# Kernel tuning notes

Hardware: AMD Instinct MI355X
Metric: run time of the kernel (lower is better)

## Reference

```python
import jax, jax.numpy as jnp
import numpy as np

C_CURV = 0.001
L = 10
N = 16
OMEGA = 1.0
EPS = 1e-6


def _fnmap(x, a0, a, b):
    # x: [M, C]; radial Fourier gate
    r = jnp.maximum(jnp.linalg.norm(x, axis=1, keepdims=True), EPS)  # [M,1]
    n = jnp.arange(1, N + 1, dtype=x.dtype)[None, :]                 # [1,N]
    angle = OMEGA * (r * n)                                          # [M,N]
    f_r = a0 + jnp.cos(angle) @ a[:, None] + jnp.sin(angle) @ b[:, None]  # [M,1]
    return f_r * x


def _log_map_origin(x, c):
    sc = jnp.sqrt(c)
    rn = jnp.maximum(jnp.linalg.norm(x, axis=1, keepdims=True), EPS)
    arg = jnp.minimum(sc * rn, 1.0 - 1e-5)
    return (jnp.arctanh(arg) / (sc * rn)) * x


def _exp_map_origin(v, c):
    sc = jnp.sqrt(c)
    rn = jnp.maximum(jnp.linalg.norm(v, axis=1, keepdims=True), EPS)
    return (jnp.tanh(sc * rn) / (sc * rn)) * v


def setup_inputs() -> dict:
    key = jax.random.key(0)
    ks = jax.random.split(key, 8)
    B, C, H, W = 32, 256, 64, 64
    x = jax.random.normal(ks[0], (B, C, H, W), dtype=jnp.float32) * 0.1
    inp = {
        "x": x,
        "a0_1": jnp.ones((1,), jnp.float32),
        "a_1": jax.random.normal(ks[1], (N,), jnp.float32) * 0.02,
        "b_1": jax.random.normal(ks[2], (N,), jnp.float32) * 0.02,
        "a0_2": jnp.ones((1,), jnp.float32),
        "a_2": jax.random.normal(ks[3], (N,), jnp.float32) * 0.02,
        "b_2": jax.random.normal(ks[4], (N,), jnp.float32) * 0.02,
        "phi": jax.random.normal(ks[5], (C,), jnp.float32) * 0.02,
        "alpha": jnp.ones((1,), jnp.float32),
        "beta": jnp.zeros((1,), jnp.float32),
    }
    return inp


def reference(x, a0_1, a_1, b_1, a0_2, a_2, b_2, phi, alpha, beta):
    B, C, H, W = x.shape
    h0 = jnp.transpose(x, (0, 2, 3, 1)).reshape(-1, C)  # [B*H*W, C]
    u = _log_map_origin(h0, C_CURV)
    u1 = _fnmap(u, a0_1, a_1, b_1)
    U = jnp.fft.rfft(u1, axis=1)                         # [M, C//2+1]
    ang = L * phi
    Hf = jax.lax.complex(jnp.cos(ang), jnp.sin(ang))     # [C]
    V = U * Hf[None, : U.shape[-1]]
    v0 = jnp.fft.irfft(V, n=C, axis=1)
    v1 = _fnmap(v0, a0_2, a_2, b_2)
    y = _exp_map_origin(v1, C_CURV)
    out = alpha * y + beta * h0
    return jnp.transpose(out.reshape(B, H, W, C), (0, 3, 1, 2))
```

## Files before the change

### kernel.cpp

```cpp
#include <hip/hip_runtime.h>
#include <math.h>

typedef __attribute__((ext_vector_type(8))) unsigned short ushort8;
typedef __attribute__((ext_vector_type(8))) __bf16 bf16x8;
typedef __attribute__((ext_vector_type(4))) float f32x4;

constexpr int   CDIM  = 256;
constexpr int   HWSP  = 4096;
constexpr int   PPB   = 64;
constexpr float SQRTC = 0.031622776601683794f;
constexpr float EPSR  = 1e-6f;

__device__ inline unsigned short f2bf(float x) {
    unsigned int u = __float_as_uint(x);
    u += 0x7FFFu + ((u >> 16) & 1u);
    return (unsigned short)(u >> 16);
}
__device__ inline float bf2f(unsigned short v) {
    return __uint_as_float(((unsigned int)v) << 16);
}

__global__ void build_w_kernel(const float* __restrict__ phi,
                               float* __restrict__ w) {
    const int d = threadIdx.x;
    const float step = 6.283185307179586f / 256.0f;
    double s = 0.0;
    for (int k = 1; k <= 127; ++k) {
        int kd = (k * d) & 255;
        float ang = 10.0f * phi[k] + step * (float)kd;
        s += 2.0 * (double)cosf(ang);
    }
    s += (double)cosf(10.0f * phi[0]);
    double c128 = (double)cosf(10.0f * phi[128]);
    s += (d & 1) ? -c128 : c128;
    w[d] = (float)(s * (1.0 / 256.0));
}

__global__ void build_wbf_kernel(const float* __restrict__ w,
                                 unsigned short* __restrict__ wbf) {
    const int j = blockIdx.x;
    const int c = threadIdx.x;
    wbf[j * CDIM + c] = f2bf(w[(j - c) & 255]);
}

__device__ inline float fourier_gate(float r, float A0,
                                     const float* __restrict__ a,
                                     const float* __restrict__ b) {
    float sn, cs;
    sincosf(r, &sn, &cs);
    float c = cs, s = sn, f = A0;
    #pragma unroll
    for (int n = 0; n < 16; ++n) {
        f = fmaf(a[n], c, f);
        f = fmaf(b[n], s, f);
        float c2 = fmaf(c, cs, -s * sn);
        float s2 = fmaf(s, cs,  c * sn);
        c = c2; s = s2;
    }
    return f;
}

__global__ __launch_bounds__(256, 3)
void fused_mfma(const float* __restrict__ x,
                const float* __restrict__ a0_1, const float* __restrict__ a1,
                const float* __restrict__ b1,
                const float* __restrict__ a0_2, const float* __restrict__ a2,
                const float* __restrict__ b2,
                const float* __restrict__ alpha, const float* __restrict__ beta,
                const unsigned short* __restrict__ wbf,
                float* __restrict__ out) {
    __shared__ __align__(16) unsigned short Xl[PPB][CDIM];
    __shared__ float ns[4][PPB];
    __shared__ float sc2[4][PPB];
    __shared__ float s1buf[PPB];
    __shared__ float sobuf[PPB];

    const int t  = threadIdx.x;
    const int l  = t & 63;
    const int g  = t >> 6;
    const int b  = blockIdx.x >> 6;
    const int s0 = (blockIdx.x & 63) * PPB;
    const float* xb = x + (size_t)b * CDIM * HWSP + s0;

    {
        const int p   = l;
        const int swz = (p & 7) << 3;
        float n0sq = 0.f;
        #pragma unroll
        for (int k = 0; k < 8; ++k) {
            const int ch0 = (g + 4 * k) * 8;
            float v[8];
            #pragma unroll
            for (int j = 0; j < 8; ++j)
                v[j] = xb[(size_t)(ch0 + j) * HWSP + p];
            ushort8 u;
            #pragma unroll
            for (int j = 0; j < 8; ++j) {
                n0sq = fmaf(v[j], v[j], n0sq);
                u[j] = f2bf(v[j]);
            }
            *reinterpret_cast<ushort8*>(&Xl[p][ch0 ^ swz]) = u;
        }
        ns[g][p] = n0sq;
    }
    __syncthreads();

    if (t < PPB) {
        float nsq = ns[0][t] + ns[1][t] + ns[2][t] + ns[3][t];
        float n0  = sqrtf(nsq);
        float rn0 = fmaxf(n0, EPSR);
        float arg = fminf(SQRTC * rn0, 1.0f - 1e-5f);
        float ls  = atanhf(arg) / (SQRTC * rn0);
        float r1  = fmaxf(ls * n0, EPSR);
        s1buf[t]  = ls * fourier_gate(r1, a0_1[0], a1, b1);
    }

    const int lr = l & 15;
    const int lk = l >> 4;
    const int jbase = g * 64;
    f32x4 acc[4][4];
    #pragma unroll
    for (int m = 0; m < 4; ++m)
        #pragma unroll
        for (int n = 0; n < 4; ++n)
            acc[m][n] = f32x4{0.f, 0.f, 0.f, 0.f};

    #pragma unroll
    for (int ks = 0; ks < 8; ++ks) {
        const int kb = ks * 32 + lk * 8;
        bf16x8 af[4], bfr[4];
        #pragma unroll
        for (int m = 0; m < 4; ++m) {
            const int row = jbase + m * 16 + lr;
            af[m] = __builtin_bit_cast(bf16x8,
                *reinterpret_cast<const ushort8*>(&wbf[row * CDIM + kb]));
        }
        #pragma unroll
        for (int n = 0; n < 4; ++n) {
            const int pos = n * 16 + lr;
            const int ch  = kb ^ ((pos & 7) << 3);
            bfr[n] = __builtin_bit_cast(bf16x8,
                *reinterpret_cast<const ushort8*>(&Xl[pos][ch]));
        }
        #pragma unroll
        for (int m = 0; m < 4; ++m)
            #pragma unroll
            for (int n = 0; n < 4; ++n)
                acc[m][n] = __builtin_amdgcn_mfma_f32_16x16x32_bf16(
                    af[m], bfr[n], acc[m][n], 0, 0, 0);
    }

    {
        float part[4];
        #pragma unroll
        for (int n = 0; n < 4; ++n) {
            float s = 0.f;
            #pragma unroll
            for (int m = 0; m < 4; ++m)
                #pragma unroll
                for (int r = 0; r < 4; ++r)
                    s = fmaf(acc[m][n][r], acc[m][n][r], s);
            s += __shfl_xor(s, 16, 64);
            s += __shfl_xor(s, 32, 64);
            part[n] = s;
        }
        if (lk == 0) {
            #pragma unroll
            for (int n = 0; n < 4; ++n) sc2[g][n * 16 + lr] = part[n];
        }
    }
    __syncthreads();

    if (t < PPB) {
        float nvsq = sc2[0][t] + sc2[1][t] + sc2[2][t] + sc2[3][t];
        float s1   = s1buf[t];
        float nv   = sqrtf(nvsq) * fabsf(s1);
        float r2   = fmaxf(nv, EPSR);
        float f2   = fourier_gate(r2, a0_2[0], a2, b2);
        float rn1  = fmaxf(fabsf(f2) * nv, EPSR);
        float es   = tanhf(SQRTC * rn1) / (SQRTC * rn1);
        sobuf[t]   = alpha[0] * es * f2 * s1;
    }
    __syncthreads();

    const float bb = beta[0];
    float* ob = out + (size_t)b * CDIM * HWSP + s0;
    if (bb == 0.f) {
        #pragma unroll
        for (int m = 0; m < 4; ++m)
            #pragma unroll
            for (int r = 0; r < 4; ++r)
                #pragma unroll
                for (int n = 0; n < 4; ++n) {
                    const int row = jbase + m * 16 + lk * 4 + r;
                    const int pos = n * 16 + lr;
                    ob[(size_t)row * HWSP + pos] = sobuf[pos] * acc[m][n][r];
                }
    } else {
        #pragma unroll
        for (int m = 0; m < 4; ++m)
            #pragma unroll
            for (int r = 0; r < 4; ++r)
                #pragma unroll
                for (int n = 0; n < 4; ++n) {
                    const int row = jbase + m * 16 + lk * 4 + r;
                    const int pos = n * 16 + lr;
                    const float h0 = bf2f(Xl[pos][row ^ ((pos & 7) << 3)]);
                    ob[(size_t)row * HWSP + pos] =
                        fmaf(bb, h0, sobuf[pos] * acc[m][n][r]);
                }
    }
}

extern "C" void kernel_launch(void* const* d_in, const int* in_sizes, int n_in,
                              void* d_out, int out_size, void* d_ws, size_t ws_size,
                              hipStream_t stream) {
    const float* x     = (const float*)d_in[0];
    const float* a0_1  = (const float*)d_in[1];
    const float* a1    = (const float*)d_in[2];
    const float* b1    = (const float*)d_in[3];
    const float* a0_2  = (const float*)d_in[4];
    const float* a2    = (const float*)d_in[5];
    const float* b2    = (const float*)d_in[6];
    const float* phi   = (const float*)d_in[7];
    const float* alpha = (const float*)d_in[8];
    const float* beta  = (const float*)d_in[9];

    float*          wtab = (float*)d_ws;
    unsigned short* wbf  = (unsigned short*)((char*)d_ws + 1024);

    build_w_kernel<<<1, 256, 0, stream>>>(phi, wtab);
    build_wbf_kernel<<<CDIM, CDIM, 0, stream>>>(wtab, wbf);

    const int B = in_sizes[0] / (CDIM * HWSP);
    fused_mfma<<<dim3(B * (HWSP / PPB)), dim3(256), 0, stream>>>(
        x, a0_1, a1, b1, a0_2, a2, b2, alpha, beta, wbf, (float*)d_out);
}
```

Measured before the change: 93.30 us.

## Compute spectral-filter output norm analytically and vectorize loads/stores with packed weights

New measurement: 81.86 us. 1.14x faster.

```diff
diff --git a/kernel.cpp b/kernel.cpp
--- a/kernel.cpp
+++ b/kernel.cpp
@@ -16,31 +16,34 @@
     u += 0x7FFFu + ((u >> 16) & 1u);
     return (unsigned short)(u >> 16);
 }
-__device__ inline float bf2f(unsigned short v) {
-    return __uint_as_float(((unsigned int)v) << 16);
-}
-
-__global__ void build_w_kernel(const float* __restrict__ phi,
-                               float* __restrict__ w) {
+
+__global__ void build_wpk(const float* __restrict__ phi,
+                          unsigned short* __restrict__ wpk) {
+    __shared__ float w[256];
     const int d = threadIdx.x;
-    const float step = 6.283185307179586f / 256.0f;
-    double s = 0.0;
-    for (int k = 1; k <= 127; ++k) {
-        int kd = (k * d) & 255;
-        float ang = 10.0f * phi[k] + step * (float)kd;
-        s += 2.0 * (double)cosf(ang);
-    }
-    s += (double)cosf(10.0f * phi[0]);
-    double c128 = (double)cosf(10.0f * phi[128]);
-    s += (d & 1) ? -c128 : c128;
-    w[d] = (float)(s * (1.0 / 256.0));
-}
-
-__global__ void build_wbf_kernel(const float* __restrict__ w,
-                                 unsigned short* __restrict__ wbf) {
-    const int j = blockIdx.x;
-    const int c = threadIdx.x;
-    wbf[j * CDIM + c] = f2bf(w[(j - c) & 255]);
+    {
+        const float step = 6.283185307179586f / 256.0f;
+        double s = 0.0;
+        for (int k = 1; k <= 127; ++k) {
+            int kd = (k * d) & 255;
+            s += 2.0 * (double)cosf(10.0f * phi[k] + step * (float)kd);
+        }
+        s += (double)cosf(10.0f * phi[0]);
+        double c128 = (double)cosf(10.0f * phi[128]);
+        s += (d & 1) ? -c128 : c128;
+        w[d] = (float)(s * (1.0 / 256.0));
+    }
+    __syncthreads();
+    const int l = d & 63, q = d >> 6;
+    for (int blk = q; blk < 128; blk += 4) {
+        const int outc = (blk & 15) * 16 + (l & 15);
+        const int ch0  = (blk >> 4) * 32 + (l >> 4) * 8;
+        ushort8 u;
+        #pragma unroll
+        for (int j = 0; j < 8; ++j)
+            u[j] = f2bf(w[(outc - (ch0 + j)) & 255]);
+        *reinterpret_cast<ushort8*>(&wpk[(size_t)(blk * 64 + l) * 8]) = u;
+    }
 }
 
 __device__ inline float fourier_gate(float r, float A0,
@@ -60,64 +63,91 @@
     return f;
 }
 
-__global__ __launch_bounds__(256, 3)
+__global__ __launch_bounds__(256, 4)
 void fused_mfma(const float* __restrict__ x,
                 const float* __restrict__ a0_1, const float* __restrict__ a1,
                 const float* __restrict__ b1,
                 const float* __restrict__ a0_2, const float* __restrict__ a2,
                 const float* __restrict__ b2,
+                const float* __restrict__ phi,
                 const float* __restrict__ alpha, const float* __restrict__ beta,
-                const unsigned short* __restrict__ wbf,
+                const unsigned short* __restrict__ wpk,
                 float* __restrict__ out) {
     __shared__ __align__(16) unsigned short Xl[PPB][CDIM];
-    __shared__ float ns[4][PPB];
-    __shared__ float sc2[4][PPB];
-    __shared__ float s1buf[PPB];
-    __shared__ float sobuf[PPB];
+    __shared__ __align__(16) float stats[3][4][PPB];
+    __shared__ __align__(16) float sobuf[PPB];
 
     const int t  = threadIdx.x;
     const int l  = t & 63;
     const int g  = t >> 6;
+    const int lr = l & 15;
+    const int lk = l >> 4;
     const int b  = blockIdx.x >> 6;
     const int s0 = (blockIdx.x & 63) * PPB;
     const float* xb = x + (size_t)b * CDIM * HWSP + s0;
 
-    {
-        const int p   = l;
-        const int swz = (p & 7) << 3;
-        float n0sq = 0.f;
-        #pragma unroll
-        for (int k = 0; k < 8; ++k) {
-            const int ch0 = (g + 4 * k) * 8;
-            float v[8];
-            #pragma unroll
-            for (int j = 0; j < 8; ++j)
-                v[j] = xb[(size_t)(ch0 + j) * HWSP + p];
+    f32x4 vns = {0.f,0.f,0.f,0.f}, vs0 = {0.f,0.f,0.f,0.f}, vsa = {0.f,0.f,0.f,0.f};
+    const int posq = t & 15;
+    #pragma unroll
+    for (int i = 0; i < 2; ++i) {
+        const int co = i * 16 + (t >> 4);
+        f32x4 v[8];
+        #pragma unroll
+        for (int j = 0; j < 8; ++j)
+            v[j] = *reinterpret_cast<const f32x4*>(
+                       &xb[(size_t)(co * 8 + j) * HWSP + posq * 4]);
+        #pragma unroll
+        for (int j = 0; j < 8; ++j) {
+            vns += v[j] * v[j];
+            vs0 += v[j];
+            vsa  = (j & 1) ? vsa - v[j] : vsa + v[j];
+        }
+        #pragma unroll
+        for (int r = 0; r < 4; ++r) {
             ushort8 u;
             #pragma unroll
-            for (int j = 0; j < 8; ++j) {
-                n0sq = fmaf(v[j], v[j], n0sq);
-                u[j] = f2bf(v[j]);
-            }
-            *reinterpret_cast<ushort8*>(&Xl[p][ch0 ^ swz]) = u;
-        }
-        ns[g][p] = n0sq;
+            for (int j = 0; j < 8; ++j) u[j] = f2bf(v[j][r]);
+            const int pos = posq * 4 + r;
+            *reinterpret_cast<ushort8*>(&Xl[pos][(co * 8) ^ ((pos & 15) << 3)]) = u;
+        }
+    }
+    #pragma unroll
+    for (int r = 0; r < 4; ++r) {
+        float aa = vns[r], ss = vs0[r], mm = vsa[r];
+        aa += __shfl_xor(aa, 16, 64); aa += __shfl_xor(aa, 32, 64);
+        ss += __shfl_xor(ss, 16, 64); ss += __shfl_xor(ss, 32, 64);
+        mm += __shfl_xor(mm, 16, 64); mm += __shfl_xor(mm, 32, 64);
+        vns[r] = aa; vs0[r] = ss; vsa[r] = mm;
+    }
+    if (lk == 0) {
+        *reinterpret_cast<f32x4*>(&stats[0][g][posq * 4]) = vns;
+        *reinterpret_cast<f32x4*>(&stats[1][g][posq * 4]) = vs0;
+        *reinterpret_cast<f32x4*>(&stats[2][g][posq * 4]) = vsa;
     }
     __syncthreads();
 
     if (t < PPB) {
-        float nsq = ns[0][t] + ns[1][t] + ns[2][t] + ns[3][t];
+        float nsq = stats[0][0][t] + stats[0][1][t] + stats[0][2][t] + stats[0][3][t];
+        float S0  = stats[1][0][t] + stats[1][1][t] + stats[1][2][t] + stats[1][3][t];
+        float Sa  = stats[2][0][t] + stats[2][1][t] + stats[2][2][t] + stats[2][3][t];
+        float sin0 = sinf(10.0f * phi[0]);
+        float sinN = sinf(10.0f * phi[128]);
         float n0  = sqrtf(nsq);
         float rn0 = fmaxf(n0, EPSR);
         float arg = fminf(SQRTC * rn0, 1.0f - 1e-5f);
         float ls  = atanhf(arg) / (SQRTC * rn0);
         float r1  = fmaxf(ls * n0, EPSR);
-        s1buf[t]  = ls * fourier_gate(r1, a0_1[0], a1, b1);
-    }
-
-    const int lr = l & 15;
-    const int lk = l >> 4;
-    const int jbase = g * 64;
+        float s1  = ls * fourier_gate(r1, a0_1[0], a1, b1);
+        float dn2 = fmaxf(nsq - (S0 * S0 * sin0 * sin0 + Sa * Sa * sinN * sinN)
+                                 * (1.0f / 256.0f), 0.f);
+        float nv  = sqrtf(dn2) * fabsf(s1);
+        float r2  = fmaxf(nv, EPSR);
+        float f2  = fourier_gate(r2, a0_2[0], a2, b2);
+        float rn1 = fmaxf(fabsf(f2) * nv, EPSR);
+        float es  = tanhf(SQRTC * rn1) / (SQRTC * rn1);
+        sobuf[t]  = alpha[0] * es * f2 * s1;
+    }
+
     f32x4 acc[4][4];
     #pragma unroll
     for (int m = 0; m < 4; ++m)
@@ -128,58 +158,24 @@
     #pragma unroll
     for (int ks = 0; ks < 8; ++ks) {
         const int kb = ks * 32 + lk * 8;
-        bf16x8 af[4], bfr[4];
+        bf16x8 af[4], bw[4];
         #pragma unroll
         for (int m = 0; m < 4; ++m) {
-            const int row = jbase + m * 16 + lr;
+            const int pos = m * 16 + lr;
             af[m] = __builtin_bit_cast(bf16x8,
-                *reinterpret_cast<const ushort8*>(&wbf[row * CDIM + kb]));
-        }
-        #pragma unroll
-        for (int n = 0; n < 4; ++n) {
-            const int pos = n * 16 + lr;
-            const int ch  = kb ^ ((pos & 7) << 3);
-            bfr[n] = __builtin_bit_cast(bf16x8,
-                *reinterpret_cast<const ushort8*>(&Xl[pos][ch]));
-        }
+                *reinterpret_cast<const ushort8*>(&Xl[pos][kb ^ ((pos & 15) << 3)]));
+        }
+        #pragma unroll
+        for (int n = 0; n < 4; ++n)
+            bw[n] = __builtin_bit_cast(bf16x8,
+                *reinterpret_cast<const ushort8*>(
+                    &wpk[(size_t)((ks * 16 + g * 4 + n) * 64 + l) * 8]));
         #pragma unroll
         for (int m = 0; m < 4; ++m)
             #pragma unroll
             for (int n = 0; n < 4; ++n)
                 acc[m][n] = __builtin_amdgcn_mfma_f32_16x16x32_bf16(
-                    af[m], bfr[n], acc[m][n], 0, 0, 0);
-    }
-
-    {
-        float part[4];
-        #pragma unroll
-        for (int n = 0; n < 4; ++n) {
-            float s = 0.f;
-            #pragma unroll
-            for (int m = 0; m < 4; ++m)
-                #pragma unroll
-                for (int r = 0; r < 4; ++r)
-                    s = fmaf(acc[m][n][r], acc[m][n][r], s);
-            s += __shfl_xor(s, 16, 64);
-            s += __shfl_xor(s, 32, 64);
-            part[n] = s;
-        }
-        if (lk == 0) {
-            #pragma unroll
-            for (int n = 0; n < 4; ++n) sc2[g][n * 16 + lr] = part[n];
-        }
-    }
-    __syncthreads();
-
-    if (t < PPB) {
-        float nvsq = sc2[0][t] + sc2[1][t] + sc2[2][t] + sc2[3][t];
-        float s1   = s1buf[t];
-        float nv   = sqrtf(nvsq) * fabsf(s1);
-        float r2   = fmaxf(nv, EPSR);
-        float f2   = fourier_gate(r2, a0_2[0], a2, b2);
-        float rn1  = fmaxf(fabsf(f2) * nv, EPSR);
-        float es   = tanhf(SQRTC * rn1) / (SQRTC * rn1);
-        sobuf[t]   = alpha[0] * es * f2 * s1;
+                    af[m], bw[n], acc[m][n], 0, 0, 0);
     }
     __syncthreads();
 
@@ -187,28 +183,30 @@
     float* ob = out + (size_t)b * CDIM * HWSP + s0;
     if (bb == 0.f) {
         #pragma unroll
-        for (int m = 0; m < 4; ++m)
-            #pragma unroll
-            for (int r = 0; r < 4; ++r)
-                #pragma unroll
-                for (int n = 0; n < 4; ++n) {
-                    const int row = jbase + m * 16 + lk * 4 + r;
-                    const int pos = n * 16 + lr;
-                    ob[(size_t)row * HWSP + pos] = sobuf[pos] * acc[m][n][r];
-                }
+        for (int m = 0; m < 4; ++m) {
+            const int p0 = m * 16 + lk * 4;
+            const f32x4 sob = *reinterpret_cast<const f32x4*>(&sobuf[p0]);
+            #pragma unroll
+            for (int n = 0; n < 4; ++n) {
+                const int outc = (g * 4 + n) * 16 + lr;
+                f32x4 vv = acc[m][n] * sob;
+                *reinterpret_cast<f32x4*>(&ob[(size_t)outc * HWSP + p0]) = vv;
+            }
+        }
     } else {
         #pragma unroll
-        for (int m = 0; m < 4; ++m)
-            #pragma unroll
-            for (int r = 0; r < 4; ++r)
-                #pragma unroll
-                for (int n = 0; n < 4; ++n) {
-                    const int row = jbase + m * 16 + lk * 4 + r;
-                    const int pos = n * 16 + lr;
-                    const float h0 = bf2f(Xl[pos][row ^ ((pos & 7) << 3)]);
-                    ob[(size_t)row * HWSP + pos] =
-                        fmaf(bb, h0, sobuf[pos] * acc[m][n][r]);
-                }
+        for (int m = 0; m < 4; ++m) {
+            const int p0 = m * 16 + lk * 4;
+            const f32x4 sob = *reinterpret_cast<const f32x4*>(&sobuf[p0]);
+            #pragma unroll
+            for (int n = 0; n < 4; ++n) {
+                const int outc = (g * 4 + n) * 16 + lr;
+                const f32x4 xv = *reinterpret_cast<const f32x4*>(
+                                     &xb[(size_t)outc * HWSP + p0]);
+                f32x4 vv = acc[m][n] * sob + bb * xv;
+                *reinterpret_cast<f32x4*>(&ob[(size_t)outc * HWSP + p0]) = vv;
+            }
+        }
     }
 }
 
@@ -226,13 +224,11 @@
     const float* alpha = (const float*)d_in[8];
     const float* beta  = (const float*)d_in[9];
 
-    float*          wtab = (float*)d_ws;
-    unsigned short* wbf  = (unsigned short*)((char*)d_ws + 1024);
-
-    build_w_kernel<<<1, 256, 0, stream>>>(phi, wtab);
-    build_wbf_kernel<<<CDIM, CDIM, 0, stream>>>(wtab, wbf);
+    unsigned short* wpk = (unsigned short*)d_ws;
+
+    build_wpk<<<1, 256, 0, stream>>>(phi, wpk);
 
     const int B = in_sizes[0] / (CDIM * HWSP);
     fused_mfma<<<dim3(B * (HWSP / PPB)), dim3(256), 0, stream>>>(
-        x, a0_1, a1, b1, a0_2, a2, b2, alpha, beta, wbf, (float*)d_out);
-}
+        x, a0_1, a1, b1, a0_2, a2, b2, phi, alpha, beta, wpk, (float*)d_out);
+}
```
